# Optimization experiments

Hardware: AMD Instinct MI355X
Metric: run time of the kernel (lower is better)

The kernel has to match this reference:

```python
import jax, jax.numpy as jnp
import numpy as np

N = 50000      # nodes
E = 1600000    # edges (before self-loops)
IN = 128       # in_chnl
H = 2          # heads
C = 64         # out_chnl per head
NEG_SLOPE = 0.2


def setup_inputs() -> dict:
    key = jax.random.key(0)
    k1, k2, k3, k4, k5 = jax.random.split(key, 5)
    h_node = jax.random.normal(k1, (N, IN), dtype=jnp.float32)
    edge_index = jax.random.randint(k2, (2, E), 0, N, dtype=jnp.int32)
    s = 1.0 / np.sqrt(IN)
    W = (jax.random.normal(k3, (IN, H * C), dtype=jnp.float32) * s)
    att_src = jax.random.normal(k4, (H, C), dtype=jnp.float32) * s
    att_dst = jax.random.normal(k5, (H, C), dtype=jnp.float32) * s
    bias = jnp.zeros((H * C,), dtype=jnp.float32)
    return {"h_node": h_node, "edge_index": edge_index, "W": W,
            "att_src": att_src, "att_dst": att_dst, "bias": bias}


def reference(h_node, edge_index, W, att_src, att_dst, bias):
    # dropout is identity in eval mode
    src, dst = edge_index[0], edge_index[1]
    # PyG GATConv default: add self-loops
    loops = jnp.arange(N, dtype=src.dtype)
    src = jnp.concatenate([src, loops])
    dst = jnp.concatenate([dst, loops])

    x = (h_node @ W).reshape(N, H, C)              # [N,H,C] projected features
    a_s = jnp.sum(x * att_src, axis=-1)            # [N,H] source attention terms
    a_d = jnp.sum(x * att_dst, axis=-1)            # [N,H] dest attention terms

    e = jax.nn.leaky_relu(a_s[src] + a_d[dst], NEG_SLOPE)        # [E+N,H]
    # segment softmax over edges grouped by destination node
    m = jax.lax.stop_gradient(jax.ops.segment_max(e, dst, num_segments=N))
    ex = jnp.exp(e - m[dst])
    den = jax.ops.segment_sum(ex, dst, num_segments=N)           # [N,H]
    alpha = ex / den[dst]                                        # [E+N,H]

    out = jax.ops.segment_sum(alpha[:, :, None] * x[src], dst, num_segments=N)
    out = out.reshape(N, H * C) + bias             # concat=True -> [N, H*C]
    return jax.nn.elu(out)
```

## Files before the change

kernel.cpp:

```cpp
#include <hip/hip_runtime.h>
#include <hip/hip_fp16.h>

#define NN 50000
#define EE 1600000
#define TOT (EE + NN)
#define INC 128
#define HC 128
#define NEG_SLOPE 0.2f

#define EPB 4096
#define NB1 ((TOT + EPB - 1) / EPB)
#define RNG 128
#define NR ((NN + RNG - 1) / RNG)
#define CAPR 4864
#define NPB 4
#define MAXD 136
#define PROJB ((NN + 63) / 64)

__device__ __forceinline__ unsigned short f2h(float f) {
    __half h = __float2half(f);
    return __half_as_ushort(h);
}

#define LOADW(dst, kk)                                                        \
    _Pragma("unroll") for (int q = 0; q < 4; q++) {                           \
        float4 wv4 = *reinterpret_cast<const float4*>(&W[(size_t)((kk) + q) * HC + j2 * 4]); \
        dst[q][0] = wv4.x; dst[q][1] = wv4.y; dst[q][2] = wv4.z; dst[q][3] = wv4.w; \
    }

#define FMAS(wv, kk)                                                          \
    _Pragma("unroll") for (int r8 = 0; r8 < 8; r8++) {                        \
        const float* hr = hs + (rg * 8 + r8) * INC + (kk);                    \
        float4 hv = *reinterpret_cast<const float4*>(hr);                     \
        _Pragma("unroll") for (int c = 0; c < 4; c++)                         \
            acc[r8][c] += hv.x * wv[0][c] + hv.y * wv[1][c]                   \
                        + hv.z * wv[2][c] + hv.w * wv[3][c];                  \
    }

__device__ __forceinline__ void proj_body(
        char* smem, int pb,
        const float* __restrict__ h, const float* __restrict__ W,
        const float* __restrict__ att_src, const float* __restrict__ att_dst,
        unsigned short* __restrict__ x_h,
        float* __restrict__ a_s, float* __restrict__ a_d) {
    float* hs = (float*)smem;
    const int t = threadIdx.x;
    const int row0 = pb * 64;

    for (int q = t; q < 64 * 32; q += 256) {
        int rr = q >> 5;
        int c4 = (q & 31) << 2;
        int gr = row0 + rr;
        float4 v = (gr < NN) ? *reinterpret_cast<const float4*>(&h[(size_t)gr * INC + c4])
                             : make_float4(0.f, 0.f, 0.f, 0.f);
        *reinterpret_cast<float4*>(&hs[rr * INC + c4]) = v;
    }
    __syncthreads();

    const int j2 = t & 31;
    const int rg = t >> 5;
    float acc[8][4];
#pragma unroll
    for (int r8 = 0; r8 < 8; r8++)
#pragma unroll
        for (int c = 0; c < 4; c++) acc[r8][c] = 0.f;

    float wA[4][4], wB[4][4];
    LOADW(wA, 0)
    for (int k = 0; k < INC; k += 8) {
        LOADW(wB, k + 4)
        FMAS(wA, k)
        if (k + 8 < INC) { LOADW(wA, k + 8) }
        FMAS(wB, k + 4)
    }

#pragma unroll
    for (int r8 = 0; r8 < 8; r8++) {
        int gr = row0 + rg * 8 + r8;
        if (gr < NN) {
            ushort4 sv;
            sv.x = f2h(acc[r8][0]);
            sv.y = f2h(acc[r8][1]);
            sv.z = f2h(acc[r8][2]);
            sv.w = f2h(acc[r8][3]);
            *reinterpret_cast<ushort4*>(&x_h[(size_t)gr * HC + j2 * 4]) = sv;
        }
    }

    const int lane = t & 63;
    const int hidx = j2 >> 4;
    const float4 avs = *reinterpret_cast<const float4*>(&att_src[j2 * 4]);
    const float4 avd = *reinterpret_cast<const float4*>(&att_dst[j2 * 4]);
#pragma unroll
    for (int r8 = 0; r8 < 8; r8++) {
        float ps = acc[r8][0] * avs.x + acc[r8][1] * avs.y
                 + acc[r8][2] * avs.z + acc[r8][3] * avs.w;
        float pd = acc[r8][0] * avd.x + acc[r8][1] * avd.y
                 + acc[r8][2] * avd.z + acc[r8][3] * avd.w;
#pragma unroll
        for (int o = 1; o < 16; o <<= 1) {
            ps += __shfl_xor(ps, o);
            pd += __shfl_xor(pd, o);
        }
        int gr = row0 + rg * 8 + r8;
        if ((lane & 15) == 0 && gr < NN) {
            a_s[gr * 2 + hidx] = ps;
            a_d[gr * 2 + hidx] = pd;
        }
    }
}

__device__ __forceinline__ void bin_body(
        char* smem, int b,
        const int* __restrict__ ei,
        unsigned int* __restrict__ gbin, unsigned short* __restrict__ bofs) {
    int* cnt = (int*)smem;
    int* ofs = cnt + NR;
    int* cur = ofs + NR + 1;
    int* wsum = cur + NR;
    unsigned int* lbuf = (unsigned int*)(wsum + 4);
    const int t = threadIdx.x;

    for (int i = t; i < NR; i += 256) cnt[i] = 0;
    __syncthreads();

    unsigned int pk[16];
    bool vd[16];
#pragma unroll
    for (int q = 0; q < 16; q++) {
        int i = b * EPB + q * 256 + t;
        vd[q] = (i < TOT);
        int s, d;
        if (i < EE)       { s = ei[i]; d = ei[EE + i]; }
        else if (i < TOT) { s = d = i - EE; }
        else              { s = d = 0; }
        pk[q] = ((unsigned int)(d >> 7) << 23) |
                ((unsigned int)(d & 127) << 16) | (unsigned int)s;
        if (vd[q]) atomicAdd(&cnt[pk[q] >> 23], 1);
    }
    __syncthreads();

    {
        int v0 = (2 * t < NR) ? cnt[2 * t] : 0;
        int v1 = (2 * t + 1 < NR) ? cnt[2 * t + 1] : 0;
        int ps = v0 + v1;
        int sc = ps;
        int lane = t & 63, wid = t >> 6;
#pragma unroll
        for (int o = 1; o < 64; o <<= 1) {
            int u = __shfl_up(sc, o);
            if (lane >= o) sc += u;
        }
        if (lane == 63) wsum[wid] = sc;
        __syncthreads();
        int woff = 0;
        for (int ww = 0; ww < wid; ww++) woff += wsum[ww];
        int excl = woff + sc - ps;
        if (2 * t <= NR) ofs[2 * t] = excl;
        if (2 * t < NR) cur[2 * t] = excl;
        if (2 * t + 1 <= NR) ofs[2 * t + 1] = excl + v0;
        if (2 * t + 1 < NR) cur[2 * t + 1] = excl + v0;
    }
    __syncthreads();

#pragma unroll
    for (int q = 0; q < 16; q++) {
        if (vd[q]) {
            int pos = atomicAdd(&cur[pk[q] >> 23], 1);
            lbuf[pos] = pk[q];
        }
    }
    __syncthreads();

#pragma unroll
    for (int q = 0; q < 16; q++)
        gbin[(size_t)b * EPB + q * 256 + t] = lbuf[q * 256 + t];
    for (int i = t; i <= NR; i += 256)
        bofs[(size_t)b * (NR + 1) + i] = (unsigned short)ofs[i];
}

__global__ __launch_bounds__(256) void gat_fused1(
        const float* __restrict__ h, const float* __restrict__ W,
        const float* __restrict__ att_src, const float* __restrict__ att_dst,
        const int* __restrict__ ei,
        unsigned int* __restrict__ gbin, unsigned short* __restrict__ bofs,
        unsigned short* __restrict__ x_h,
        float* __restrict__ a_s, float* __restrict__ a_d) {
    __shared__ __align__(16) char smem[64 * INC * 4];
    if (blockIdx.x < NB1)
        bin_body(smem, blockIdx.x, ei, gbin, bofs);
    else
        proj_body(smem, blockIdx.x - NB1, h, W, att_src, att_dst, x_h, a_s, a_d);
}

__global__ __launch_bounds__(512) void gat_build2(
        const unsigned int* __restrict__ gbin,
        const unsigned short* __restrict__ bofs,
        unsigned short* __restrict__ csr,
        int* __restrict__ start32,
        int* __restrict__ deg32) {
    __shared__ unsigned int est[CAPR];
    __shared__ int sbase[512];
    __shared__ int segofs[NB1];
    __shared__ int deg[RNG];
    __shared__ int ofs[RNG + 1];
    __shared__ int cur[RNG];
    __shared__ int wsum[8];
    __shared__ int tot_sh;
    const int t = threadIdx.x;
    const int r = blockIdx.x;
    const int lane = t & 63, wid = t >> 6;

    int c = 0;
    if (t < NB1) {
        int o0 = (int)bofs[(size_t)t * (NR + 1) + r];
        int o1 = (int)bofs[(size_t)t * (NR + 1) + r + 1];
        c = o1 - o0;
        segofs[t] = o0;
    }
    int sc = c;
#pragma unroll
    for (int o = 1; o < 64; o <<= 1) {
        int u = __shfl_up(sc, o);
        if (lane >= o) sc += u;
    }
    if (lane == 63) wsum[wid] = sc;
    if (t < RNG) { deg[t] = 0; cur[t] = 0; }
    __syncthreads();
    int woff = 0;
    for (int ww = 0; ww < wid; ww++) woff += wsum[ww];
    int excl = woff + sc - c;
    sbase[t] = excl;
    if (t == 511) tot_sh = excl + c;
    __syncthreads();

    const int tot = min(tot_sh, CAPR);

    for (int e = t; e < tot; e += 512) {
        int lo = 0, hi = NB1 - 1;
        while (lo < hi) {
            int mid = (lo + hi + 1) >> 1;
            if (sbase[mid] <= e) lo = mid; else hi = mid - 1;
        }
        unsigned int v = gbin[(size_t)lo * EPB + segofs[lo] + (e - sbase[lo])];
        est[e] = v;
        atomicAdd(&deg[(v >> 16) & 127], 1);
    }
    __syncthreads();

    {
        int v = (t < RNG) ? deg[t] : 0;
        if (t < 128) {
            int sc2 = v;
#pragma unroll
            for (int o = 1; o < 64; o <<= 1) {
                int u = __shfl_up(sc2, o);
                if (lane >= o) sc2 += u;
            }
            if (lane == 63) wsum[wid] = sc2;
            __syncthreads();
            int woff2 = (wid == 1) ? wsum[0] : 0;
            int excl2 = woff2 + sc2 - v;
            ofs[t] = excl2;
            if (t == 127) ofs[RNG] = excl2 + v;
        } else {
            __syncthreads();
        }
    }
    __syncthreads();

    const int rbase = r * CAPR;
    for (int i = t; i < tot; i += 512) {
        unsigned int e = est[i];
        int dl = (e >> 16) & 127;
        int pos = atomicAdd(&cur[dl], 1);
        csr[(size_t)rbase + ofs[dl] + pos] = (unsigned short)(e & 0xFFFFu);
    }

    if (t < RNG) {
        int n = r * RNG + t;
        if (n < NN) {
            start32[n] = rbase + ofs[t];
            deg32[n] = deg[t];
        }
    }
}

#define ACCUM(u32v, aL, aH)                                                   \
    asm("v_fma_mix_f32 %0, %1, %2, %0 op_sel_hi:[0,1,0]"                      \
        : "+v"(aL) : "v"(wk), "v"(u32v));                                     \
    asm("v_fma_mix_f32 %0, %1, %2, %0 op_sel:[0,1,0] op_sel_hi:[0,1,0]"       \
        : "+v"(aH) : "v"(wk), "v"(u32v));

__global__ __launch_bounds__(256) void gat_aggr(
        const uint4* __restrict__ x16,
        const float2* __restrict__ a_s2, const float2* __restrict__ a_d2,
        const int* __restrict__ start32, const int* __restrict__ deg32,
        const unsigned short* __restrict__ csr,
        const float4* __restrict__ bias4, float4* __restrict__ out4) {
    __shared__ int    s_src[NPB][MAXD];
    __shared__ float2 s_p[NPB][MAXD];
    const int w    = threadIdx.x >> 6;
    const int lane = threadIdx.x & 63;
    const int n    = blockIdx.x * NPB + w;
    if (n >= NN) return;

    const int deg  = min(deg32[n], MAXD - 4);
    const int base = start32[n];
    const float2 ad = a_d2[n];

    float d0 = 0.f, d1 = 0.f;
    for (int jj = lane; jj < deg; jj += 64) {
        int s = (int)csr[(size_t)base + jj];
        s_src[w][jj] = s;
        float2 as = a_s2[s];
        float e0 = as.x + ad.x; e0 = (e0 > 0.f) ? e0 : NEG_SLOPE * e0;
        float e1 = as.y + ad.y; e1 = (e1 > 0.f) ? e1 : NEG_SLOPE * e1;
        float p0 = __expf(e0), p1 = __expf(e1);
        s_p[w][jj] = make_float2(p0, p1);
        d0 += p0;
        d1 += p1;
    }
    if (lane < 4) {
        s_src[w][deg + lane] = 0;
        s_p[w][deg + lane] = make_float2(0.f, 0.f);
    }
#pragma unroll
    for (int off = 32; off; off >>= 1) {
        d0 += __shfl_xor(d0, off);
        d1 += __shfl_xor(d1, off);
    }

    const int sub = lane >> 4;
    const int cl  = lane & 15;
    const int hd  = cl >> 3;
    const float* __restrict__ pwl = &s_p[w][0].x + hd;

    float a0=0.f,a1=0.f,a2=0.f,a3=0.f,a4=0.f,a5=0.f,a6=0.f,a7=0.f;
    const int ng = (deg + 3) >> 2;
    int g = 0;
    for (; g + 4 <= ng; g += 4) {
#pragma unroll
        for (int k = 0; k < 4; k++) {
            int e = 4 * (g + k) + sub;
            int s = s_src[w][e];
            uint4 u = x16[(size_t)s * 16 + cl];
            float wk = pwl[2 * e];
            ACCUM(u.x, a0, a1)
            ACCUM(u.y, a2, a3)
            ACCUM(u.z, a4, a5)
            ACCUM(u.w, a6, a7)
        }
    }
    for (; g < ng; g++) {
        int e = 4 * g + sub;
        int s = s_src[w][e];
        uint4 u = x16[(size_t)s * 16 + cl];
        float wk = pwl[2 * e];
        ACCUM(u.x, a0, a1)
        ACCUM(u.y, a2, a3)
        ACCUM(u.z, a4, a5)
        ACCUM(u.w, a6, a7)
    }
#define MRG(a) a += __shfl_xor(a, 16); a += __shfl_xor(a, 32);
    MRG(a0) MRG(a1) MRG(a2) MRG(a3) MRG(a4) MRG(a5) MRG(a6) MRG(a7)
#undef MRG

    if (lane < 32) {
        const int hf = lane >> 4;
        const float invd = 1.0f / (hd ? d1 : d0);
        float4 bb = bias4[cl * 2 + hf];
        float v0 = (hf ? a4 : a0) * invd + bb.x;
        float v1 = (hf ? a5 : a1) * invd + bb.y;
        float v2 = (hf ? a6 : a2) * invd + bb.z;
        float v3 = (hf ? a7 : a3) * invd + bb.w;
        v0 = (v0 > 0.f) ? v0 : __expf(v0) - 1.0f;
        v1 = (v1 > 0.f) ? v1 : __expf(v1) - 1.0f;
        v2 = (v2 > 0.f) ? v2 : __expf(v2) - 1.0f;
        v3 = (v3 > 0.f) ? v3 : __expf(v3) - 1.0f;
        out4[(size_t)n * 32 + cl * 2 + hf] = make_float4(v0, v1, v2, v3);
    }
}

static inline size_t align256(size_t v) { return (v + 255) & ~(size_t)255; }

extern "C" void kernel_launch(void* const* d_in, const int* in_sizes, int n_in,
                              void* d_out, int out_size, void* d_ws, size_t ws_size,
                              hipStream_t stream) {
    const float* h_node  = (const float*)d_in[0];
    const int*   ei      = (const int*)d_in[1];
    const float* W       = (const float*)d_in[2];
    const float* att_src = (const float*)d_in[3];
    const float* att_dst = (const float*)d_in[4];
    const float* bias    = (const float*)d_in[5];
    float* out = (float*)d_out;

    char* base = (char*)d_ws;
    size_t off = 0;
    unsigned short* x_h = (unsigned short*)(base + off);
    off = align256(off + (size_t)NN * HC * 2);
    float* a_s = (float*)(base + off);      off = align256(off + (size_t)NN * 2 * 4);
    float* a_d = (float*)(base + off);      off = align256(off + (size_t)NN * 2 * 4);
    unsigned int* gbin = (unsigned int*)(base + off);
    off = align256(off + (size_t)NB1 * EPB * 4);
    unsigned short* bofs = (unsigned short*)(base + off);
    off = align256(off + (size_t)NB1 * (NR + 1) * 2);
    unsigned short* csr = (unsigned short*)(base + off);
    off = align256(off + (size_t)NR * CAPR * 2);
    int* start32 = (int*)(base + off);      off = align256(off + (size_t)NN * 4);
    int* deg32 = (int*)(base + off);        off = align256(off + (size_t)NN * 4);
    (void)ws_size;

    gat_fused1<<<NB1 + PROJB, 256, 0, stream>>>(h_node, W, att_src, att_dst, ei,
                                                gbin, bofs, x_h, a_s, a_d);
    gat_build2<<<NR, 512, 0, stream>>>(gbin, bofs, csr, start32, deg32);
    gat_aggr<<<(NN + NPB - 1) / NPB, 256, 0, stream>>>((const uint4*)x_h,
                                                       (const float2*)a_s,
                                                       (const float2*)a_d,
                                                       start32, deg32, csr,
                                                       (const float4*)bias,
                                                       (float4*)out);
}
```

Measured before the change: 192.0 us.

## Fuse CSR build and aggregation into one per-range LDS kernel

Merges the CSR-building kernel and the aggregation kernel into a single kernel. Each block gathers the binned edges for 64 destination nodes, computes the unnormalised attention weights, and sorts edges by destination in LDS. It then aggregates features for those nodes directly. This removes the global CSR, start and degree arrays and one kernel launch, and stores the per-edge exp weights packed as fp16. The trade-offs are coarser parallelism (one 512-thread block per 64 nodes), a larger LDS footprint, a fixed per-range edge capacity, and reduced precision of the attention weights.

```diff
diff --git a/kernel.cpp b/kernel.cpp
--- a/kernel.cpp
+++ b/kernel.cpp
@@ -10,16 +10,22 @@
 
 #define EPB 4096
 #define NB1 ((TOT + EPB - 1) / EPB)
-#define RNG 128
-#define NR ((NN + RNG - 1) / RNG)
-#define CAPR 4864
-#define NPB 4
-#define MAXD 136
+#define RNG2 64
+#define NR2 ((NN + RNG2 - 1) / RNG2)
+#define CAPR2 2624
+#define PADC (CAPR2 + 4 * RNG2)
 #define PROJB ((NN + 63) / 64)
 
 __device__ __forceinline__ unsigned short f2h(float f) {
     __half h = __float2half(f);
     return __half_as_ushort(h);
+}
+
+__device__ __forceinline__ unsigned int packp(float a, float b) {
+    typedef __fp16 h2 __attribute__((ext_vector_type(2)));
+    union { h2 h; unsigned int u; } cv;
+    cv.h = __builtin_amdgcn_cvt_pkrtz(a, b);
+    return cv.u;
 }
 
 #define LOADW(dst, kk)                                                        \
@@ -115,13 +121,13 @@
         const int* __restrict__ ei,
         unsigned int* __restrict__ gbin, unsigned short* __restrict__ bofs) {
     int* cnt = (int*)smem;
-    int* ofs = cnt + NR;
-    int* cur = ofs + NR + 1;
-    int* wsum = cur + NR;
+    int* ofs = cnt + NR2;
+    int* cur = ofs + NR2 + 1;
+    int* wsum = cur + NR2;
     unsigned int* lbuf = (unsigned int*)(wsum + 4);
     const int t = threadIdx.x;
 
-    for (int i = t; i < NR; i += 256) cnt[i] = 0;
+    for (int i = t; i < NR2; i += 256) cnt[i] = 0;
     __syncthreads();
 
     unsigned int pk[16];
@@ -134,16 +140,19 @@
         if (i < EE)       { s = ei[i]; d = ei[EE + i]; }
         else if (i < TOT) { s = d = i - EE; }
         else              { s = d = 0; }
-        pk[q] = ((unsigned int)(d >> 7) << 23) |
-                ((unsigned int)(d & 127) << 16) | (unsigned int)s;
-        if (vd[q]) atomicAdd(&cnt[pk[q] >> 23], 1);
+        pk[q] = ((unsigned int)(d >> 6) << 22) |
+                ((unsigned int)(d & 63) << 16) | (unsigned int)s;
+        if (vd[q]) atomicAdd(&cnt[pk[q] >> 22], 1);
     }
     __syncthreads();
 
     {
-        int v0 = (2 * t < NR) ? cnt[2 * t] : 0;
-        int v1 = (2 * t + 1 < NR) ? cnt[2 * t + 1] : 0;
-        int ps = v0 + v1;
+        int i0 = 4 * t;
+        int v0 = (i0     < NR2) ? cnt[i0]     : 0;
+        int v1 = (i0 + 1 < NR2) ? cnt[i0 + 1] : 0;
+        int v2 = (i0 + 2 < NR2) ? cnt[i0 + 2] : 0;
+        int v3 = (i0 + 3 < NR2) ? cnt[i0 + 3] : 0;
+        int ps = v0 + v1 + v2 + v3;
         int sc = ps;
         int lane = t & 63, wid = t >> 6;
 #pragma unroll
@@ -155,18 +164,18 @@
         __syncthreads();
         int woff = 0;
         for (int ww = 0; ww < wid; ww++) woff += wsum[ww];
-        int excl = woff + sc - ps;
-        if (2 * t <= NR) ofs[2 * t] = excl;
-        if (2 * t < NR) cur[2 * t] = excl;
-        if (2 * t + 1 <= NR) ofs[2 * t + 1] = excl + v0;
-        if (2 * t + 1 < NR) cur[2 * t + 1] = excl + v0;
+        int run = woff + sc - ps;
+        if (i0     <= NR2) ofs[i0]     = run; if (i0     < NR2) cur[i0]     = run; run += v0;
+        if (i0 + 1 <= NR2) ofs[i0 + 1] = run; if (i0 + 1 < NR2) cur[i0 + 1] = run; run += v1;
+        if (i0 + 2 <= NR2) ofs[i0 + 2] = run; if (i0 + 2 < NR2) cur[i0 + 2] = run; run += v2;
+        if (i0 + 3 <= NR2) ofs[i0 + 3] = run; if (i0 + 3 < NR2) cur[i0 + 3] = run;
     }
     __syncthreads();
 
 #pragma unroll
     for (int q = 0; q < 16; q++) {
         if (vd[q]) {
-            int pos = atomicAdd(&cur[pk[q] >> 23], 1);
+            int pos = atomicAdd(&cur[pk[q] >> 22], 1);
             lbuf[pos] = pk[q];
         }
     }
@@ -175,8 +184,8 @@
 #pragma unroll
     for (int q = 0; q < 16; q++)
         gbin[(size_t)b * EPB + q * 256 + t] = lbuf[q * 256 + t];
-    for (int i = t; i <= NR; i += 256)
-        bofs[(size_t)b * (NR + 1) + i] = (unsigned short)ofs[i];
+    for (int i = t; i <= NR2; i += 256)
+        bofs[(size_t)b * (NR2 + 1) + i] = (unsigned short)ofs[i];
 }
 
 __global__ __launch_bounds__(256) void gat_fused1(
@@ -193,28 +202,41 @@
         proj_body(smem, blockIdx.x - NB1, h, W, att_src, att_dst, x_h, a_s, a_d);
 }
 
-__global__ __launch_bounds__(512) void gat_build2(
+#define ACCUM(u32v, aL, aH)                                                   \
+    asm("v_fma_mix_f32 %0, %1, %2, %0 op_sel_hi:[0,1,0]"                      \
+        : "+v"(aL) : "v"(wk), "v"(u32v));                                     \
+    asm("v_fma_mix_f32 %0, %1, %2, %0 op_sel:[0,1,0] op_sel_hi:[0,1,0]"       \
+        : "+v"(aH) : "v"(wk), "v"(u32v));
+
+__global__ __launch_bounds__(512) void gat_ragg(
         const unsigned int* __restrict__ gbin,
         const unsigned short* __restrict__ bofs,
-        unsigned short* __restrict__ csr,
-        int* __restrict__ start32,
-        int* __restrict__ deg32) {
-    __shared__ unsigned int est[CAPR];
+        const uint4* __restrict__ x16,
+        const float2* __restrict__ a_s2, const float2* __restrict__ a_d2,
+        const float4* __restrict__ bias4, float4* __restrict__ out4) {
     __shared__ int sbase[512];
     __shared__ int segofs[NB1];
-    __shared__ int deg[RNG];
-    __shared__ int ofs[RNG + 1];
-    __shared__ int cur[RNG];
+    __shared__ unsigned short esrc[CAPR2];
+    __shared__ unsigned char  edst[CAPR2];
+    __shared__ unsigned int   pvh[CAPR2];
+    __shared__ unsigned short csrc[PADC];
+    __shared__ unsigned int   cpv[PADC];
+    __shared__ int deg[RNG2];
+    __shared__ int ofsP[RNG2];
+    __shared__ int cur[RNG2];
     __shared__ int wsum[8];
     __shared__ int tot_sh;
+
     const int t = threadIdx.x;
     const int r = blockIdx.x;
     const int lane = t & 63, wid = t >> 6;
 
+    if (t < RNG2) { deg[t] = 0; cur[t] = 0; }
+
     int c = 0;
     if (t < NB1) {
-        int o0 = (int)bofs[(size_t)t * (NR + 1) + r];
-        int o1 = (int)bofs[(size_t)t * (NR + 1) + r + 1];
+        int o0 = (int)bofs[(size_t)t * (NR2 + 1) + r];
+        int o1 = (int)bofs[(size_t)t * (NR2 + 1) + r + 1];
         c = o1 - o0;
         segofs[t] = o0;
     }
@@ -225,7 +247,6 @@
         if (lane >= o) sc += u;
     }
     if (lane == 63) wsum[wid] = sc;
-    if (t < RNG) { deg[t] = 0; cur[t] = 0; }
     __syncthreads();
     int woff = 0;
     for (int ww = 0; ww < wid; ww++) woff += wsum[ww];
@@ -233,9 +254,9 @@
     sbase[t] = excl;
     if (t == 511) tot_sh = excl + c;
     __syncthreads();
-
-    const int tot = min(tot_sh, CAPR);
-
+    const int tot = min(tot_sh, CAPR2);
+
+    const float2* __restrict__ adr = a_d2 + (size_t)r * RNG2;
     for (int e = t; e < tot; e += 512) {
         int lo = 0, hi = NB1 - 1;
         while (lo < hi) {
@@ -243,142 +264,113 @@
             if (sbase[mid] <= e) lo = mid; else hi = mid - 1;
         }
         unsigned int v = gbin[(size_t)lo * EPB + segofs[lo] + (e - sbase[lo])];
-        est[e] = v;
-        atomicAdd(&deg[(v >> 16) & 127], 1);
-    }
-    __syncthreads();
-
-    {
-        int v = (t < RNG) ? deg[t] : 0;
-        if (t < 128) {
-            int sc2 = v;
-#pragma unroll
-            for (int o = 1; o < 64; o <<= 1) {
-                int u = __shfl_up(sc2, o);
-                if (lane >= o) sc2 += u;
-            }
-            if (lane == 63) wsum[wid] = sc2;
-            __syncthreads();
-            int woff2 = (wid == 1) ? wsum[0] : 0;
-            int excl2 = woff2 + sc2 - v;
-            ofs[t] = excl2;
-            if (t == 127) ofs[RNG] = excl2 + v;
-        } else {
-            __syncthreads();
-        }
-    }
-    __syncthreads();
-
-    const int rbase = r * CAPR;
-    for (int i = t; i < tot; i += 512) {
-        unsigned int e = est[i];
-        int dl = (e >> 16) & 127;
-        int pos = atomicAdd(&cur[dl], 1);
-        csr[(size_t)rbase + ofs[dl] + pos] = (unsigned short)(e & 0xFFFFu);
-    }
-
-    if (t < RNG) {
-        int n = r * RNG + t;
-        if (n < NN) {
-            start32[n] = rbase + ofs[t];
-            deg32[n] = deg[t];
-        }
-    }
-}
-
-#define ACCUM(u32v, aL, aH)                                                   \
-    asm("v_fma_mix_f32 %0, %1, %2, %0 op_sel_hi:[0,1,0]"                      \
-        : "+v"(aL) : "v"(wk), "v"(u32v));                                     \
-    asm("v_fma_mix_f32 %0, %1, %2, %0 op_sel:[0,1,0] op_sel_hi:[0,1,0]"       \
-        : "+v"(aH) : "v"(wk), "v"(u32v));
-
-__global__ __launch_bounds__(256) void gat_aggr(
-        const uint4* __restrict__ x16,
-        const float2* __restrict__ a_s2, const float2* __restrict__ a_d2,
-        const int* __restrict__ start32, const int* __restrict__ deg32,
-        const unsigned short* __restrict__ csr,
-        const float4* __restrict__ bias4, float4* __restrict__ out4) {
-    __shared__ int    s_src[NPB][MAXD];
-    __shared__ float2 s_p[NPB][MAXD];
-    const int w    = threadIdx.x >> 6;
-    const int lane = threadIdx.x & 63;
-    const int n    = blockIdx.x * NPB + w;
-    if (n >= NN) return;
-
-    const int deg  = min(deg32[n], MAXD - 4);
-    const int base = start32[n];
-    const float2 ad = a_d2[n];
-
-    float d0 = 0.f, d1 = 0.f;
-    for (int jj = lane; jj < deg; jj += 64) {
-        int s = (int)csr[(size_t)base + jj];
-        s_src[w][jj] = s;
+        int s  = (int)(v & 0xFFFFu);
+        int dl = (int)((v >> 16) & 63u);
+        esrc[e] = (unsigned short)s;
+        edst[e] = (unsigned char)dl;
         float2 as = a_s2[s];
+        float2 ad = adr[dl];
         float e0 = as.x + ad.x; e0 = (e0 > 0.f) ? e0 : NEG_SLOPE * e0;
         float e1 = as.y + ad.y; e1 = (e1 > 0.f) ? e1 : NEG_SLOPE * e1;
-        float p0 = __expf(e0), p1 = __expf(e1);
-        s_p[w][jj] = make_float2(p0, p1);
-        d0 += p0;
-        d1 += p1;
-    }
-    if (lane < 4) {
-        s_src[w][deg + lane] = 0;
-        s_p[w][deg + lane] = make_float2(0.f, 0.f);
-    }
-#pragma unroll
-    for (int off = 32; off; off >>= 1) {
-        d0 += __shfl_xor(d0, off);
-        d1 += __shfl_xor(d1, off);
-    }
+        pvh[e] = packp(__expf(e0), __expf(e1));
+        atomicAdd(&deg[dl], 1);
+    }
+    __syncthreads();
+
+    if (t < RNG2) {
+        int v = deg[t];
+        int s2 = v;
+#pragma unroll
+        for (int o = 1; o < 64; o <<= 1) {
+            int u = __shfl_up(s2, o);
+            if (lane >= o) s2 += u;
+        }
+        ofsP[t] = (s2 - v) + 4 * t;
+    }
+    __syncthreads();
+
+    for (int e = t; e < tot; e += 512) {
+        int dl = edst[e];
+        int slot = ofsP[dl] + atomicAdd(&cur[dl], 1);
+        csrc[slot] = esrc[e];
+        cpv[slot]  = pvh[e];
+    }
+    if (t < RNG2 * 4) {
+        int j = t >> 2, q = t & 3;
+        int slot = ofsP[j] + deg[j] + q;
+        csrc[slot] = 0;
+        cpv[slot] = 0;
+    }
+    __syncthreads();
 
     const int sub = lane >> 4;
     const int cl  = lane & 15;
     const int hd  = cl >> 3;
-    const float* __restrict__ pwl = &s_p[w][0].x + hd;
-
-    float a0=0.f,a1=0.f,a2=0.f,a3=0.f,a4=0.f,a5=0.f,a6=0.f,a7=0.f;
-    const int ng = (deg + 3) >> 2;
-    int g = 0;
-    for (; g + 4 <= ng; g += 4) {
-#pragma unroll
-        for (int k = 0; k < 4; k++) {
-            int e = 4 * (g + k) + sub;
-            int s = s_src[w][e];
+    const int hsh = hd << 4;
+    for (int jl = wid; jl < RNG2; jl += 8) {
+        int n = r * RNG2 + jl;
+        if (n >= NN) continue;
+        const int dj = deg[jl];
+        const int w0 = ofsP[jl];
+
+        float d0 = 0.f, d1 = 0.f;
+        for (int jj = lane; jj < dj; jj += 64) {
+            unsigned int ph = cpv[w0 + jj];
+            d0 += __half2float(__ushort_as_half((unsigned short)ph));
+            d1 += __half2float(__ushort_as_half((unsigned short)(ph >> 16)));
+        }
+#pragma unroll
+        for (int off = 32; off; off >>= 1) {
+            d0 += __shfl_xor(d0, off);
+            d1 += __shfl_xor(d1, off);
+        }
+
+        float a0=0.f,a1=0.f,a2=0.f,a3=0.f,a4=0.f,a5=0.f,a6=0.f,a7=0.f;
+        const int ng = (dj + 3) >> 2;
+        int g = 0;
+        for (; g + 4 <= ng; g += 4) {
+#pragma unroll
+            for (int k = 0; k < 4; k++) {
+                int e = 4 * (g + k) + sub;
+                int s = (int)csrc[w0 + e];
+                unsigned int ph = cpv[w0 + e];
+                float wk = __half2float(__ushort_as_half((unsigned short)(ph >> hsh)));
+                uint4 u = x16[(size_t)s * 16 + cl];
+                ACCUM(u.x, a0, a1)
+                ACCUM(u.y, a2, a3)
+                ACCUM(u.z, a4, a5)
+                ACCUM(u.w, a6, a7)
+            }
+        }
+        for (; g < ng; g++) {
+            int e = 4 * g + sub;
+            int s = (int)csrc[w0 + e];
+            unsigned int ph = cpv[w0 + e];
+            float wk = __half2float(__ushort_as_half((unsigned short)(ph >> hsh)));
             uint4 u = x16[(size_t)s * 16 + cl];
-            float wk = pwl[2 * e];
             ACCUM(u.x, a0, a1)
             ACCUM(u.y, a2, a3)
             ACCUM(u.z, a4, a5)
             ACCUM(u.w, a6, a7)
         }
-    }
-    for (; g < ng; g++) {
-        int e = 4 * g + sub;
-        int s = s_src[w][e];
-        uint4 u = x16[(size_t)s * 16 + cl];
-        float wk = pwl[2 * e];
-        ACCUM(u.x, a0, a1)
-        ACCUM(u.y, a2, a3)
-        ACCUM(u.z, a4, a5)
-        ACCUM(u.w, a6, a7)
-    }
 #define MRG(a) a += __shfl_xor(a, 16); a += __shfl_xor(a, 32);
-    MRG(a0) MRG(a1) MRG(a2) MRG(a3) MRG(a4) MRG(a5) MRG(a6) MRG(a7)
+        MRG(a0) MRG(a1) MRG(a2) MRG(a3) MRG(a4) MRG(a5) MRG(a6) MRG(a7)
 #undef MRG
 
-    if (lane < 32) {
-        const int hf = lane >> 4;
-        const float invd = 1.0f / (hd ? d1 : d0);
-        float4 bb = bias4[cl * 2 + hf];
-        float v0 = (hf ? a4 : a0) * invd + bb.x;
-        float v1 = (hf ? a5 : a1) * invd + bb.y;
-        float v2 = (hf ? a6 : a2) * invd + bb.z;
-        float v3 = (hf ? a7 : a3) * invd + bb.w;
-        v0 = (v0 > 0.f) ? v0 : __expf(v0) - 1.0f;
-        v1 = (v1 > 0.f) ? v1 : __expf(v1) - 1.0f;
-        v2 = (v2 > 0.f) ? v2 : __expf(v2) - 1.0f;
-        v3 = (v3 > 0.f) ? v3 : __expf(v3) - 1.0f;
-        out4[(size_t)n * 32 + cl * 2 + hf] = make_float4(v0, v1, v2, v3);
+        if (lane < 32) {
+            const int hf = lane >> 4;
+            const float invd = 1.0f / (hd ? d1 : d0);
+            float4 bb = bias4[cl * 2 + hf];
+            float v0 = (hf ? a4 : a0) * invd + bb.x;
+            float v1 = (hf ? a5 : a1) * invd + bb.y;
+            float v2 = (hf ? a6 : a2) * invd + bb.z;
+            float v3 = (hf ? a7 : a3) * invd + bb.w;
+            v0 = (v0 > 0.f) ? v0 : __expf(v0) - 1.0f;
+            v1 = (v1 > 0.f) ? v1 : __expf(v1) - 1.0f;
+            v2 = (v2 > 0.f) ? v2 : __expf(v2) - 1.0f;
+            v3 = (v3 > 0.f) ? v3 : __expf(v3) - 1.0f;
+            out4[(size_t)n * 32 + cl * 2 + hf] = make_float4(v0, v1, v2, v3);
+        }
     }
 }
 
@@ -404,20 +396,12 @@
     unsigned int* gbin = (unsigned int*)(base + off);
     off = align256(off + (size_t)NB1 * EPB * 4);
     unsigned short* bofs = (unsigned short*)(base + off);
-    off = align256(off + (size_t)NB1 * (NR + 1) * 2);
-    unsigned short* csr = (unsigned short*)(base + off);
-    off = align256(off + (size_t)NR * CAPR * 2);
-    int* start32 = (int*)(base + off);      off = align256(off + (size_t)NN * 4);
-    int* deg32 = (int*)(base + off);        off = align256(off + (size_t)NN * 4);
+    off = align256(off + (size_t)NB1 * (NR2 + 1) * 2);
     (void)ws_size;
 
     gat_fused1<<<NB1 + PROJB, 256, 0, stream>>>(h_node, W, att_src, att_dst, ei,
                                                 gbin, bofs, x_h, a_s, a_d);
-    gat_build2<<<NR, 512, 0, stream>>>(gbin, bofs, csr, start32, deg32);
-    gat_aggr<<<(NN + NPB - 1) / NPB, 256, 0, stream>>>((const uint4*)x_h,
-                                                       (const float2*)a_s,
-                                                       (const float2*)a_d,
-                                                       start32, deg32, csr,
-                                                       (const float4*)bias,
-                                                       (float4*)out);
-}
+    gat_ragg<<<NR2, 512, 0, stream>>>(gbin, bofs, (const uint4*)x_h,
+                                      (const float2*)a_s, (const float2*)a_d,
+                                      (const float4*)bias, (float4*)out);
+}
```

Result: faster. 187.5 us (median of 2 runs) (-2.4%).
